# Kernel optimization log

Measured on AMD Instinct MI355X. Metric: run time of the kernel, lower is better.

Reference implementation:

```python
import jax, jax.numpy as jnp
import numpy as np

VOCAB, EMB, HIDDEN, OUT = 50000, 300, 512, 2
SEQ, BATCH = 512, 1024


def setup_inputs() -> dict:
    key = jax.random.key(0)
    k_text, k_len, k_emb, k_w1, k_b1, k_w2, k_b2 = jax.random.split(key, 7)
    text = jax.random.randint(k_text, (SEQ, BATCH), 1, VOCAB, dtype=jnp.int64 if jax.config.jax_enable_x64 else jnp.int32)
    lengths = jax.random.randint(k_len, (BATCH,), 1, SEQ + 1, dtype=text.dtype)
    emb_table = jax.random.normal(k_emb, (VOCAB, EMB), dtype=jnp.float32) * 0.1
    emb_table = emb_table.at[0].set(0.0)  # padding_idx=0 row zeroed like nn.Embedding
    W1 = jax.random.normal(k_w1, (EMB, HIDDEN), dtype=jnp.float32) * (1.0 / np.sqrt(EMB))
    b1 = jax.random.normal(k_b1, (HIDDEN,), dtype=jnp.float32) * 0.01
    W2 = jax.random.normal(k_w2, (HIDDEN, OUT), dtype=jnp.float32) * (1.0 / np.sqrt(HIDDEN))
    b2 = jax.random.normal(k_b2, (OUT,), dtype=jnp.float32) * 0.01
    return {"text": text, "lengths": lengths, "emb_table": emb_table,
            "W1": W1, "b1": b1, "W2": W2, "b2": b2}


def reference(text, lengths, emb_table, W1, b1, W2, b2):
    # text: [S, B] int; embedding lookup -> [S, B, E]
    embedded = emb_table[text]
    # masked mean over the first `lengths[b]` tokens (vectorized segment mean)
    seq = embedded.shape[0]
    mask = (jnp.arange(seq)[:, None] < lengths[None, :]).astype(embedded.dtype)  # [S, B]
    pooled = jnp.einsum('sbe,sb->be', embedded, mask) / lengths[:, None].astype(embedded.dtype)  # [B, E]
    # fc1 -> (dropout p=0, identity) -> relu -> fc2
    h = jax.nn.relu(pooled @ W1 + b1)
    return h @ W2 + b2
```

## Files before the change

kernel.cpp:

```cpp
#include <hip/hip_runtime.h>

constexpr int EMB    = 300;
constexpr int EMB4   = 75;
constexpr int HIDDEN = 512;
constexpr int SEQ    = 512;
constexpr int BATCH  = 1024;
constexpr int GB     = 4;
constexpr int NSG    = 4;

__device__ __forceinline__ float4 f4add(float4 a, float4 b) {
    return make_float4(a.x + b.x, a.y + b.y, a.z + b.z, a.w + b.w);
}

__global__ __launch_bounds__(320) void pool_kernel(
    const int* __restrict__ text,
    const int* __restrict__ lengths,
    const float* __restrict__ emb,
    float* __restrict__ part,
    int NS)
{
    const int b   = blockIdx.x;
    const int h   = blockIdx.y;
    const int len = lengths[b];
    const int chunk = (len + NS - 1) / NS;
    const int s0  = h * chunk;
    const int s1  = min(len, s0 + chunk);
    const int n   = max(0, s1 - s0);

    __shared__ int    toks[SEQ];
    __shared__ float4 red[NSG][EMB4];

    for (int t = threadIdx.x; t < n; t += 320)
        toks[t] = text[(s0 + t) * BATCH + b];
    __syncthreads();

    const int t = threadIdx.x;
    if (t < NSG * EMB4) {
        const int g = t / EMB4;
        const int c = t % EMB4;
        float4 a0 = make_float4(0.f, 0.f, 0.f, 0.f);
        float4 a1 = a0, a2 = a0, a3 = a0;
        int i = g;
        for (; i + 12 < n; i += 16) {
            const float4* r0 = (const float4*)(emb + (size_t)toks[i +  0] * EMB);
            const float4* r1 = (const float4*)(emb + (size_t)toks[i +  4] * EMB);
            const float4* r2 = (const float4*)(emb + (size_t)toks[i +  8] * EMB);
            const float4* r3 = (const float4*)(emb + (size_t)toks[i + 12] * EMB);
            a0 = f4add(a0, r0[c]);
            a1 = f4add(a1, r1[c]);
            a2 = f4add(a2, r2[c]);
            a3 = f4add(a3, r3[c]);
        }
        for (; i < n; i += 4) {
            const float4* r = (const float4*)(emb + (size_t)toks[i] * EMB);
            a0 = f4add(a0, r[c]);
        }
        red[g][c] = f4add(f4add(a0, a1), f4add(a2, a3));
    }
    __syncthreads();

    if (t < EMB4) {
        const float4 s = f4add(f4add(red[0][t], red[1][t]),
                               f4add(red[2][t], red[3][t]));
        float4* dst = (float4*)(part + ((size_t)h * BATCH + b) * EMB);
        dst[t] = s;
    }
}

__global__ __launch_bounds__(512) void mlp_kernel(
    const float* __restrict__ part,
    const int* __restrict__ lengths,
    const float* __restrict__ W1,
    const float* __restrict__ b1,
    const float* __restrict__ W2,
    const float* __restrict__ b2,
    float* __restrict__ out,
    int NS)
{
    __shared__ float pT[EMB][GB];
    __shared__ float h[GB][HIDDEN];

    const int b0  = blockIdx.x * GB;
    const int tid = threadIdx.x;

    for (int i = tid; i < EMB * GB; i += 512) {
        const int g = i / EMB;
        const int e = i - g * EMB;
        float s = 0.f;
        for (int ns = 0; ns < NS; ++ns)
            s += part[((size_t)ns * BATCH + b0 + g) * EMB + e];
        pT[e][g] = s / (float)lengths[b0 + g];
    }
    __syncthreads();

    const int j = tid;
    const float bias1 = b1[j];
    float4 acc = make_float4(bias1, bias1, bias1, bias1);
    for (int e = 0; e < EMB; e += 4) {
        const float w0 = W1[(e + 0) * HIDDEN + j];
        const float w1 = W1[(e + 1) * HIDDEN + j];
        const float w2 = W1[(e + 2) * HIDDEN + j];
        const float w3 = W1[(e + 3) * HIDDEN + j];
        const float4 p0 = *(const float4*)&pT[e + 0][0];
        const float4 p1 = *(const float4*)&pT[e + 1][0];
        const float4 p2 = *(const float4*)&pT[e + 2][0];
        const float4 p3 = *(const float4*)&pT[e + 3][0];
        acc.x += p0.x * w0 + p1.x * w1 + p2.x * w2 + p3.x * w3;
        acc.y += p0.y * w0 + p1.y * w1 + p2.y * w2 + p3.y * w3;
        acc.z += p0.z * w0 + p1.z * w1 + p2.z * w2 + p3.z * w3;
        acc.w += p0.w * w0 + p1.w * w1 + p2.w * w2 + p3.w * w3;
    }
    h[0][j] = fmaxf(acc.x, 0.f);
    h[1][j] = fmaxf(acc.y, 0.f);
    h[2][j] = fmaxf(acc.z, 0.f);
    h[3][j] = fmaxf(acc.w, 0.f);
    __syncthreads();

    const int wave = tid >> 6;
    const int lane = tid & 63;
    if (wave < GB) {
        float s0 = 0.f, s1 = 0.f;
        for (int jj = lane; jj < HIDDEN; jj += 64) {
            const float  hv = h[wave][jj];
            const float2 w  = *(const float2*)&W2[jj * 2];
            s0 += hv * w.x;
            s1 += hv * w.y;
        }
#pragma unroll
        for (int off = 32; off > 0; off >>= 1) {
            s0 += __shfl_down(s0, off);
            s1 += __shfl_down(s1, off);
        }
        if (lane == 0) {
            out[(b0 + wave) * 2 + 0] = s0 + b2[0];
            out[(b0 + wave) * 2 + 1] = s1 + b2[1];
        }
    }
}

extern "C" void kernel_launch(void* const* d_in, const int* in_sizes, int n_in,
                              void* d_out, int out_size, void* d_ws, size_t ws_size,
                              hipStream_t stream) {
    const int*   text    = (const int*)d_in[0];
    const int*   lengths = (const int*)d_in[1];
    const float* emb     = (const float*)d_in[2];
    const float* W1      = (const float*)d_in[3];
    const float* b1      = (const float*)d_in[4];
    const float* W2      = (const float*)d_in[5];
    const float* b2      = (const float*)d_in[6];
    float*       out     = (float*)d_out;
    float*       part    = (float*)d_ws;

    const size_t poolBytes = (size_t)BATCH * EMB * sizeof(float);
    const int NS = (ws_size >= 4 * poolBytes) ? 4
                 : (ws_size >= 2 * poolBytes) ? 2 : 1;

    pool_kernel<<<dim3(BATCH, NS), 320, 0, stream>>>(text, lengths, emb, part, NS);
    mlp_kernel<<<BATCH / GB, 512, 0, stream>>>(part, lengths, W1, b1, W2, b2, out, NS);
}
```

Baseline: 73.53 us.

## Transpose tokens, deepen gather unroll, raise seq splits, halve MLP batch group

A new transpose kernel makes each sequence's token ids contiguous, so the pool kernel loads them with coalesced reads instead of stride-BATCH reads. The embedding gather loop is unrolled to eight independent loads per iteration to keep more memory requests in flight. The sequence split count can rise to 8 when workspace allows, and the MLP kernel now handles 2 batch rows per block with a 10-wide inner unroll for more blocks. The cost is an extra kernel launch and a 2 MB write and read for the transposed tokens.

```diff
diff --git a/kernel.cpp b/kernel.cpp
--- a/kernel.cpp
+++ b/kernel.cpp
@@ -5,33 +5,49 @@
 constexpr int HIDDEN = 512;
 constexpr int SEQ    = 512;
 constexpr int BATCH  = 1024;
-constexpr int GB     = 4;
+constexpr int GB     = 2;
 constexpr int NSG    = 4;
 
 __device__ __forceinline__ float4 f4add(float4 a, float4 b) {
     return make_float4(a.x + b.x, a.y + b.y, a.z + b.z, a.w + b.w);
 }
 
+__global__ __launch_bounds__(256) void transpose_kernel(
+    const int* __restrict__ text, int* __restrict__ textT)
+{
+    __shared__ int tile[32][33];
+    const int s0 = blockIdx.x * 32;
+    const int b0 = blockIdx.y * 32;
+    const int tx = threadIdx.x;
+    const int ty = threadIdx.y;
+#pragma unroll
+    for (int k = 0; k < 32; k += 8)
+        tile[ty + k][tx] = text[(size_t)(s0 + ty + k) * BATCH + (b0 + tx)];
+    __syncthreads();
+#pragma unroll
+    for (int k = 0; k < 32; k += 8)
+        textT[(size_t)(b0 + ty + k) * SEQ + (s0 + tx)] = tile[tx][ty + k];
+}
+
 __global__ __launch_bounds__(320) void pool_kernel(
-    const int* __restrict__ text,
+    const int* __restrict__ textT,
     const int* __restrict__ lengths,
     const float* __restrict__ emb,
     float* __restrict__ part,
     int NS)
 {
-    const int b   = blockIdx.x;
-    const int h   = blockIdx.y;
-    const int len = lengths[b];
+    const int b     = blockIdx.x;
+    const int h     = blockIdx.y;
+    const int len   = lengths[b];
     const int chunk = (len + NS - 1) / NS;
-    const int s0  = h * chunk;
-    const int s1  = min(len, s0 + chunk);
-    const int n   = max(0, s1 - s0);
+    const int s0    = h * chunk;
+    const int n     = max(0, min(len, s0 + chunk) - s0);
 
     __shared__ int    toks[SEQ];
     __shared__ float4 red[NSG][EMB4];
 
     for (int t = threadIdx.x; t < n; t += 320)
-        toks[t] = text[(s0 + t) * BATCH + b];
+        toks[t] = textT[(size_t)b * SEQ + s0 + t];
     __syncthreads();
 
     const int t = threadIdx.x;
@@ -41,19 +57,27 @@
         float4 a0 = make_float4(0.f, 0.f, 0.f, 0.f);
         float4 a1 = a0, a2 = a0, a3 = a0;
         int i = g;
-        for (; i + 12 < n; i += 16) {
-            const float4* r0 = (const float4*)(emb + (size_t)toks[i +  0] * EMB);
-            const float4* r1 = (const float4*)(emb + (size_t)toks[i +  4] * EMB);
-            const float4* r2 = (const float4*)(emb + (size_t)toks[i +  8] * EMB);
-            const float4* r3 = (const float4*)(emb + (size_t)toks[i + 12] * EMB);
-            a0 = f4add(a0, r0[c]);
-            a1 = f4add(a1, r1[c]);
-            a2 = f4add(a2, r2[c]);
-            a3 = f4add(a3, r3[c]);
+        for (; i + 28 < n; i += 32) {
+            const float4 v0 = ((const float4*)(emb + (size_t)toks[i +  0] * EMB))[c];
+            const float4 v1 = ((const float4*)(emb + (size_t)toks[i +  4] * EMB))[c];
+            const float4 v2 = ((const float4*)(emb + (size_t)toks[i +  8] * EMB))[c];
+            const float4 v3 = ((const float4*)(emb + (size_t)toks[i + 12] * EMB))[c];
+            const float4 v4 = ((const float4*)(emb + (size_t)toks[i + 16] * EMB))[c];
+            const float4 v5 = ((const float4*)(emb + (size_t)toks[i + 20] * EMB))[c];
+            const float4 v6 = ((const float4*)(emb + (size_t)toks[i + 24] * EMB))[c];
+            const float4 v7 = ((const float4*)(emb + (size_t)toks[i + 28] * EMB))[c];
+            a0 = f4add(a0, v0);
+            a1 = f4add(a1, v1);
+            a2 = f4add(a2, v2);
+            a3 = f4add(a3, v3);
+            a0 = f4add(a0, v4);
+            a1 = f4add(a1, v5);
+            a2 = f4add(a2, v6);
+            a3 = f4add(a3, v7);
         }
         for (; i < n; i += 4) {
-            const float4* r = (const float4*)(emb + (size_t)toks[i] * EMB);
-            a0 = f4add(a0, r[c]);
+            const float4 v = ((const float4*)(emb + (size_t)toks[i] * EMB))[c];
+            a0 = f4add(a0, v);
         }
         red[g][c] = f4add(f4add(a0, a1), f4add(a2, a3));
     }
@@ -77,43 +101,54 @@
     float* __restrict__ out,
     int NS)
 {
-    __shared__ float pT[EMB][GB];
-    __shared__ float h[GB][HIDDEN];
+    __shared__ float2 pT[EMB];
+    __shared__ float  h[GB][HIDDEN];
 
     const int b0  = blockIdx.x * GB;
     const int tid = threadIdx.x;
 
+    float* pTf = (float*)pT;
     for (int i = tid; i < EMB * GB; i += 512) {
         const int g = i / EMB;
         const int e = i - g * EMB;
         float s = 0.f;
         for (int ns = 0; ns < NS; ++ns)
             s += part[((size_t)ns * BATCH + b0 + g) * EMB + e];
-        pT[e][g] = s / (float)lengths[b0 + g];
+        pTf[e * GB + g] = s / (float)lengths[b0 + g];
     }
     __syncthreads();
 
     const int j = tid;
     const float bias1 = b1[j];
-    float4 acc = make_float4(bias1, bias1, bias1, bias1);
-    for (int e = 0; e < EMB; e += 4) {
+    float2 acc = make_float2(bias1, bias1);
+    for (int e = 0; e < EMB; e += 10) {
         const float w0 = W1[(e + 0) * HIDDEN + j];
         const float w1 = W1[(e + 1) * HIDDEN + j];
         const float w2 = W1[(e + 2) * HIDDEN + j];
         const float w3 = W1[(e + 3) * HIDDEN + j];
-        const float4 p0 = *(const float4*)&pT[e + 0][0];
-        const float4 p1 = *(const float4*)&pT[e + 1][0];
-        const float4 p2 = *(const float4*)&pT[e + 2][0];
-        const float4 p3 = *(const float4*)&pT[e + 3][0];
-        acc.x += p0.x * w0 + p1.x * w1 + p2.x * w2 + p3.x * w3;
-        acc.y += p0.y * w0 + p1.y * w1 + p2.y * w2 + p3.y * w3;
-        acc.z += p0.z * w0 + p1.z * w1 + p2.z * w2 + p3.z * w3;
-        acc.w += p0.w * w0 + p1.w * w1 + p2.w * w2 + p3.w * w3;
+        const float w4 = W1[(e + 4) * HIDDEN + j];
+        const float w5 = W1[(e + 5) * HIDDEN + j];
+        const float w6 = W1[(e + 6) * HIDDEN + j];
+        const float w7 = W1[(e + 7) * HIDDEN + j];
+        const float w8 = W1[(e + 8) * HIDDEN + j];
+        const float w9 = W1[(e + 9) * HIDDEN + j];
+        const float2 p0 = pT[e + 0];
+        const float2 p1 = pT[e + 1];
+        const float2 p2 = pT[e + 2];
+        const float2 p3 = pT[e + 3];
+        const float2 p4 = pT[e + 4];
+        const float2 p5 = pT[e + 5];
+        const float2 p6 = pT[e + 6];
+        const float2 p7 = pT[e + 7];
+        const float2 p8 = pT[e + 8];
+        const float2 p9 = pT[e + 9];
+        acc.x += p0.x * w0 + p1.x * w1 + p2.x * w2 + p3.x * w3 + p4.x * w4
+               + p5.x * w5 + p6.x * w6 + p7.x * w7 + p8.x * w8 + p9.x * w9;
+        acc.y += p0.y * w0 + p1.y * w1 + p2.y * w2 + p3.y * w3 + p4.y * w4
+               + p5.y * w5 + p6.y * w6 + p7.y * w7 + p8.y * w8 + p9.y * w9;
     }
     h[0][j] = fmaxf(acc.x, 0.f);
     h[1][j] = fmaxf(acc.y, 0.f);
-    h[2][j] = fmaxf(acc.z, 0.f);
-    h[3][j] = fmaxf(acc.w, 0.f);
     __syncthreads();
 
     const int wave = tid >> 6;
@@ -149,12 +184,17 @@
     const float* W2      = (const float*)d_in[5];
     const float* b2      = (const float*)d_in[6];
     float*       out     = (float*)d_out;
-    float*       part    = (float*)d_ws;
-
+
+    int*   textT = (int*)d_ws;
+    const size_t textBytes = (size_t)SEQ * BATCH * sizeof(int);
+    float* part  = (float*)((char*)d_ws + textBytes);
     const size_t poolBytes = (size_t)BATCH * EMB * sizeof(float);
-    const int NS = (ws_size >= 4 * poolBytes) ? 4
-                 : (ws_size >= 2 * poolBytes) ? 2 : 1;
-
-    pool_kernel<<<dim3(BATCH, NS), 320, 0, stream>>>(text, lengths, emb, part, NS);
+    const size_t avail = (ws_size > textBytes) ? ws_size - textBytes : 0;
+    const int NS = (avail >= 8 * poolBytes) ? 8
+                 : (avail >= 4 * poolBytes) ? 4
+                 : (avail >= 2 * poolBytes) ? 2 : 1;
+
+    transpose_kernel<<<dim3(SEQ / 32, BATCH / 32), dim3(32, 8), 0, stream>>>(text, textT);
+    pool_kernel<<<dim3(BATCH, NS), 320, 0, stream>>>(textT, lengths, emb, part, NS);
     mlp_kernel<<<BATCH / GB, 512, 0, stream>>>(part, lengths, W1, b1, W2, b2, out, NS);
 }
```

Measured after the change: 77.83 us. 5.8% more time.
